# Optimization experiments

Measured on AMD Instinct MI355X. Metric: run time of the kernel, lower is better.

Reference implementation:

```python
import jax, jax.numpy as jnp
import numpy as np

NUM_HEADS = 8
ALPHA = 4.0
KSIZE = 5


def _pow_relu(x, p):
    # relu(x) ** p, safe for x<=0 (avoids 0**p grad NaNs wrt p)
    pos = x > 0
    xs = jnp.where(pos, x, 1.0)
    return jnp.where(pos, xs ** p, 0.0)


def setup_inputs() -> dict:
    key = jax.random.key(0)
    ks = jax.random.split(key, 10)
    B, N, C = 16, 3136, 512
    hd = C // NUM_HEADS
    s = 0.02
    return {
        "x": jax.random.normal(ks[0], (B, N, C), jnp.float32),
        "qg_w": jax.random.normal(ks[1], (C, 2 * C), jnp.float32) * s,
        "kv_w": jax.random.normal(ks[2], (C, 2 * C), jnp.float32) * s,
        "proj_w": jax.random.normal(ks[3], (C, C), jnp.float32) * s,
        "proj_b": jax.random.normal(ks[4], (C,), jnp.float32) * s,
        "pos_enc": jax.random.normal(ks[5], (1, N, C), jnp.float32) * s,
        "scale_p": jax.random.normal(ks[6], (1, 1, C), jnp.float32) * s,
        "power_p": jax.random.normal(ks[7], (1, NUM_HEADS, 1, hd), jnp.float32) * s,
        "dwc_w": jax.random.normal(ks[8], (hd, 1, KSIZE, KSIZE), jnp.float32) * s,
        "dwc_b": jax.random.normal(ks[9], (hd,), jnp.float32) * s,
        "H": 56,
        "W": 56,
    }


def _forward(x, qg_w, kv_w, proj_w, proj_b, pos_enc, scale_p, power_p, dwc_w, dwc_b, H, W):
    B, N, C = x.shape
    nh = NUM_HEADS
    hd = C // nh
    n = N  # sr_ratio == 1

    qg = x @ qg_w                      # [B,N,2C]
    q, g = qg[..., :C], qg[..., C:]
    kv = x @ kv_w                      # [B,N,2C]
    k, v = kv[..., :C], kv[..., C:]
    k = k + pos_enc

    scale = jax.nn.softplus(scale_p)   # [1,1,C]
    q = q / scale
    k = k / scale

    def heads(t):  # [B,N,C] -> [B,nh,N,hd]
        return t.reshape(B, -1, nh, hd).transpose(0, 2, 1, 3)

    q, k, v = heads(q), heads(k), heads(v)

    power = 1.0 + ALPHA * jax.nn.sigmoid(power_p)  # [1,nh,1,hd]
    q_pos = _pow_relu(q, power)
    q_neg = _pow_relu(-q, power)
    q_sim = jnp.concatenate([q_pos, q_neg], -1)    # [B,nh,N,2hd]
    q_opp = jnp.concatenate([q_neg, q_pos], -1)
    kf = jnp.concatenate([_pow_relu(k, power), _pow_relu(-k, power)], -1)  # [B,nh,n,2hd]

    v1, v2 = kf.shape[-1] // 4, None  # v chunks below
    v1, v2 = jnp.split(v, 2, axis=-1)               # each [B,nh,n,hd/2]

    km = kf.mean(axis=2)                            # [B,nh,2hd]
    inv_n = 1.0 / n

    def branch(qf, vv):
        z = 1.0 / (jnp.einsum('bhnd,bhd->bhn', qf, km) + 1e-6)
        kv_ = jnp.einsum('bhnd,bhne->bhde', kf, vv) * inv_n   # (n^-0.5)*(n^-0.5)
        return jnp.einsum('bhnd,bhde->bhne', qf, kv_) * z[..., None]

    x_sim = branch(q_sim, v1)
    x_opp = branch(q_opp, v2)
    xo = jnp.concatenate([x_sim, x_opp], -1)        # [B,nh,N,hd]
    xo = xo.transpose(0, 2, 1, 3).reshape(B, N, C)

    # depthwise conv residual on v
    vimg = v.reshape(B * nh, H, W, hd).transpose(0, 3, 1, 2)  # [B*nh,hd,H,W]
    pad = KSIZE // 2
    vd = jax.lax.conv_general_dilated(
        vimg, dwc_w, window_strides=(1, 1), padding=((pad, pad), (pad, pad)),
        feature_group_count=hd) + dwc_b[None, :, None, None]
    vd = vd.reshape(B, C, N).transpose(0, 2, 1)     # [B,N,C]

    out = (xo + vd) * g
    return out @ proj_w + proj_b


def reference(x, qg_w, kv_w, proj_w, proj_b, pos_enc, scale_p, power_p, dwc_w, dwc_b, H, W):
    return _forward(x, qg_w, kv_w, proj_w, proj_b, pos_enc, scale_p, power_p, dwc_w, dwc_b, H, W)
```

## Files before the change

kernel.cpp:

```cpp
#include <hip/hip_runtime.h>
#include <math.h>

typedef unsigned short ushort;
typedef __attribute__((ext_vector_type(8))) short short8v;
typedef __attribute__((ext_vector_type(4))) short short4v;
typedef __attribute__((ext_vector_type(4))) float float4v;
typedef __attribute__((ext_vector_type(8))) __bf16 bf16x8;

#define NHEADS 8
#define NPOS 3136
#define MROWS 50176
#define KDIM 512

__device__ __forceinline__ ushort f2bf(float f) {
  union { float f; unsigned u; } x; x.f = f;
  unsigned r = x.u + 0x7fffu + ((x.u >> 16) & 1u);
  return (ushort)(r >> 16);
}
__device__ __forceinline__ float bf2f(ushort h) {
  union { unsigned u; float f; } x; x.u = ((unsigned)h) << 16; return x.f;
}

__device__ __forceinline__ float4v mfma16(short8v a, short8v b, float4v c) {
  return __builtin_amdgcn_mfma_f32_16x16x32_bf16(
      __builtin_bit_cast(bf16x8, a), __builtin_bit_cast(bf16x8, b), c, 0, 0, 0);
}

__device__ __forceinline__ void glds16(const void* g, void* l) {
  __builtin_amdgcn_global_load_lds(
      (const __attribute__((address_space(1))) unsigned int*)g,
      (__attribute__((address_space(3))) unsigned int*)l, 16, 0, 0);
}

__device__ __forceinline__ float fexp2(float x) {
  float r; asm("v_exp_f32 %0, %1" : "=v"(r) : "v"(x)); return r;
}
__device__ __forceinline__ float flog2(float x) {
  float r; asm("v_log_f32 %0, %1" : "=v"(r) : "v"(x)); return r;
}

__global__ __launch_bounds__(512) void prep_kernel(const float* __restrict__ scale_p,
                                                   const float* __restrict__ power_p,
                                                   float* __restrict__ scinv,
                                                   float* __restrict__ pwr)
{
  int t = threadIdx.x;
  if (t < KDIM) {
    scinv[t] = 1.f / log1pf(expf(scale_p[t]));
    pwr[t]   = 1.f + 4.f / (1.f + expf(-power_p[t]));
  }
}

__global__ __launch_bounds__(256) void cvt_x_kernel(const float* __restrict__ x,
                                                    ushort* __restrict__ xb)
{
  const size_t i = ((size_t)blockIdx.x * 256 + threadIdx.x) * 4;
  float4v v = *(const float4v*)(x + i);
  short4v o = { (short)f2bf(v[0]), (short)f2bf(v[1]), (short)f2bf(v[2]), (short)f2bf(v[3]) };
  *(short4v*)(xb + i) = o;
}

__global__ __launch_bounds__(256) void transpose_w_kernel(const float* __restrict__ src,
                                                          ushort* __restrict__ dst,
                                                          int K, int N)
{
  __shared__ float tile[32][33];
  const int t = threadIdx.x, tx = t & 31, ty = t >> 5;
  const int nb = blockIdx.x * 32, kb = blockIdx.y * 32;
  #pragma unroll
  for (int i = 0; i < 4; i++)
    tile[ty + i*8][tx] = src[(size_t)(kb + ty + i*8) * N + nb + tx];
  __syncthreads();
  #pragma unroll
  for (int i = 0; i < 4; i++)
    dst[(size_t)(nb + ty + i*8) * K + kb + tx] = f2bf(tile[tx][ty + i*8]);
}

__global__ __launch_bounds__(256) void transpose_pe_kernel(const float* __restrict__ src,
                                                           float* __restrict__ dst)
{
  __shared__ float tile[32][33];
  const int t = threadIdx.x, tx = t & 31, ty = t >> 5;
  const int nb = blockIdx.x * 32, kb = blockIdx.y * 32;
  #pragma unroll
  for (int i = 0; i < 4; i++)
    tile[ty + i*8][tx] = src[(size_t)(kb + ty + i*8) * 512 + nb + tx];
  __syncthreads();
  #pragma unroll
  for (int i = 0; i < 4; i++)
    dst[(size_t)(nb + ty + i*8) * NPOS + kb + tx] = tile[tx][ty + i*8];
}

__global__ __launch_bounds__(512, 6) void gemm_bf16_kernel(
    const ushort* __restrict__ A, const ushort* __restrict__ Bt, int mode,
    const float* __restrict__ scinv, const float* __restrict__ pwr,
    const float* __restrict__ pos_enc, const float* __restrict__ bias,
    float* __restrict__ outf, ushort* __restrict__ outb0, ushort* __restrict__ outb1,
    int nbx_shift)
{
  __shared__ ushort As[3][128*32];
  __shared__ ushort Bs[3][128*32];
  const int t = threadIdx.x;
  const int wave = t >> 6, lane = t & 63;

  const int nwg = (int)(gridDim.x * gridDim.y);
  const int lid = (int)(blockIdx.y * gridDim.x + blockIdx.x);
  const int nlid = (lid & 7) * (nwg >> 3) + (lid >> 3);
  const int bx = nlid & ((1 << nbx_shift) - 1);
  const int by = nlid >> nbx_shift;
  const int m0 = ((mode == 3) ? bx : by) * 128;
  const int n0 = ((mode == 3) ? by : bx) * 128;

  const int wm = wave >> 2, wn = wave & 3;
  const int lm = lane & 15, q = lane >> 4;

  const int srow = t >> 2;
  const int lc = ((t & 3) ^ (srow & 3) ^ ((srow >> 2) & 3)) * 8;
  const ushort* gA = A  + (size_t)(m0 + srow) * KDIM + lc;
  const ushort* gB = Bt + (size_t)(n0 + srow) * KDIM + lc;

  const int pc = (q ^ (lm & 3) ^ ((lm >> 2) & 3)) * 8;
  const int arow = wm * 64 + lm;
  const int brow = wn * 32 + lm;

  float4v acc[4][2];
  #pragma unroll
  for (int i = 0; i < 4; i++)
    #pragma unroll
    for (int j = 0; j < 2; j++) { float4v z = {0.f,0.f,0.f,0.f}; acc[i][j] = z; }

  glds16(gA,      &As[0][t*8]);
  glds16(gB,      &Bs[0][t*8]);
  glds16(gA + 32, &As[1][t*8]);
  glds16(gB + 32, &Bs[1][t*8]);

  #pragma unroll
  for (int kt = 0; kt < 16; kt++) {
    if (kt < 15) asm volatile("s_waitcnt vmcnt(2)" ::: "memory");
    else         asm volatile("s_waitcnt vmcnt(0)" ::: "memory");
    __builtin_amdgcn_sched_barrier(0);
    __builtin_amdgcn_s_barrier();
    if (kt + 2 < 16) {
      const int nb = (kt + 2) % 3;
      glds16(gA + (kt + 2) * 32, &As[nb][t*8]);
      glds16(gB + (kt + 2) * 32, &Bs[nb][t*8]);
    }
    const int cb = kt % 3;
    short8v a[4], b[2];
    #pragma unroll
    for (int i = 0; i < 4; i++)
      a[i] = *(const short8v*)&As[cb][(arow + i*16) * 32 + pc];
    #pragma unroll
    for (int j = 0; j < 2; j++)
      b[j] = *(const short8v*)&Bs[cb][(brow + j*16) * 32 + pc];
    __builtin_amdgcn_s_setprio(1);
    #pragma unroll
    for (int i = 0; i < 4; i++)
      #pragma unroll
      for (int j = 0; j < 2; j++)
        acc[i][j] = mfma16(a[i], b[j], acc[i][j]);
    __builtin_amdgcn_s_setprio(0);
  }

  const int rq = (lane >> 4) * 4;
  if (mode == 3) {
    #pragma unroll
    for (int i = 0; i < 4; i++) {
      const int of0 = m0 + wm * 64 + i * 16 + rq;
      #pragma unroll
      for (int j = 0; j < 2; j++) {
        const int gn = n0 + wn * 32 + j * 16;
        const int bb = gn / NPOS;
        const int nn = gn - bb * NPOS + lm;
        #pragma unroll
        for (int r = 0; r < 4; r++) {
          const int o = of0 + r;
          const float val = acc[i][j][r];
          if (o < 512) {
            const int h = o >> 6, d = o & 63;
            const float sv = (val + pos_enc[(size_t)o * NPOS + nn]) * scinv[o];
            const float pw = pwr[o];
            const float aq = fabsf(sv);
            const float f = fexp2(pw * flog2(aq));
            const ushort fb = f2bf(f);
            ushort* kr = outb0 + ((size_t)((bb << 3) + h) * 128 + 2 * d) * NPOS + nn;
            kr[0]    = (sv > 0.f) ? fb : (ushort)0;
            kr[NPOS] = (sv < 0.f) ? fb : (ushort)0;
          } else {
            const int ov = o - 512;
            const int h = ov >> 6, e = ov & 63;
            outb1[((size_t)((bb << 3) + h) * 64 + e) * NPOS + nn] = f2bf(val);
          }
        }
      }
    }
  } else {
    #pragma unroll
    for (int i = 0; i < 4; i++) {
      #pragma unroll
      for (int r = 0; r < 4; r++) {
        const int grow = m0 + wm * 64 + i * 16 + rq + r;
        const int bb = grow / NPOS;
        const int nn = grow - bb * NPOS;
        #pragma unroll
        for (int j = 0; j < 2; j++) {
          const int gcol = n0 + wn * 32 + j * 16 + lm;
          const float val = acc[i][j][r];
          if (mode == 2) {
            outf[(size_t)grow * 512 + gcol] = val + bias[gcol];
          } else if (gcol < 512) {
            const float sv = val * scinv[gcol];
            const float pw = pwr[gcol];
            const float aq = fabsf(sv);
            const float f = fexp2(pw * flog2(aq));
            const unsigned fb = (unsigned)f2bf(f);
            unsigned pack = 0;
            if (sv > 0.f)      pack = fb;
            else if (sv < 0.f) pack = fb << 16;
            const int h = gcol >> 6, d = gcol & 63;
            unsigned* qrow = (unsigned*)(outb0 + (((size_t)((bb << 3) + h) * NPOS + nn) << 7));
            qrow[d] = pack;
          } else {
            const int c2 = gcol - 512;
            outb1[(size_t)grow * 512 + c2] = f2bf(val);
          }
        }
      }
    }
  }
}

#define RSPLIT 7
#define RK 448
__global__ __launch_bounds__(256, 4) void reduce_kv_kernel(
    const ushort* __restrict__ KFt, const ushort* __restrict__ Vt,
    float* __restrict__ pkv, float* __restrict__ pkm)
{
  __shared__ ushort As[3][128*32];
  __shared__ ushort Bs[3][64*32];
  const int sp = blockIdx.x, bh = blockIdx.y;
  const int t = threadIdx.x;
  const int wave = t >> 6, lane = t & 63;
  const int wm = wave >> 1, wn = wave & 1;
  const int lm = lane & 15, q = lane >> 4;

  const int r0 = t >> 2;
  const int lc = ((t & 3) ^ (r0 & 3) ^ ((r0 >> 2) & 3)) * 8;
  const ushort* gA = KFt + ((size_t)bh * 128 + r0) * NPOS + sp * RK + lc;
  const ushort* gB = Vt  + ((size_t)bh * 64  + r0) * NPOS + sp * RK + lc;
  const size_t A64 = (size_t)64 * NPOS;

  const int pc = (q ^ (lm & 3) ^ ((lm >> 2) & 3)) * 8;
  const int arow = wm * 64 + lm;
  const int brow = wn * 32 + lm;

  float4v acc[4][2], accK[4];
  #pragma unroll
  for (int i = 0; i < 4; i++) {
    #pragma unroll
    for (int j = 0; j < 2; j++) { float4v z = {0.f,0.f,0.f,0.f}; acc[i][j] = z; }
    float4v z = {0.f,0.f,0.f,0.f}; accK[i] = z;
  }
  short8v bk;
  #pragma unroll
  for (int c = 0; c < 8; c++) bk[c] = (short)((lm == 0) ? 0x3F80 : 0);

  glds16(gA,            &As[0][t*8]);
  glds16(gA + A64,      &As[0][2048 + t*8]);
  glds16(gB,            &Bs[0][t*8]);
  glds16(gA + 32,       &As[1][t*8]);
  glds16(gA + A64 + 32, &As[1][2048 + t*8]);
  glds16(gB + 32,       &Bs[1][t*8]);

  #pragma unroll
  for (int kt = 0; kt < 14; kt++) {
    if (kt < 13) asm volatile("s_waitcnt vmcnt(3)" ::: "memory");
    else         asm volatile("s_waitcnt vmcnt(0)" ::: "memory");
    __builtin_amdgcn_sched_barrier(0);
    __builtin_amdgcn_s_barrier();
    if (kt + 2 < 14) {
      const int nb = (kt + 2) % 3;
      const int off = (kt + 2) * 32;
      glds16(gA + off,       &As[nb][t*8]);
      glds16(gA + A64 + off, &As[nb][2048 + t*8]);
      glds16(gB + off,       &Bs[nb][t*8]);
    }
    const int cb = kt % 3;
    short8v a[4], b[2];
    #pragma unroll
    for (int i = 0; i < 4; i++)
      a[i] = *(const short8v*)&As[cb][(arow + i*16) * 32 + pc];
    #pragma unroll
    for (int j = 0; j < 2; j++)
      b[j] = *(const short8v*)&Bs[cb][(brow + j*16) * 32 + pc];
    #pragma unroll
    for (int i = 0; i < 4; i++)
      #pragma unroll
      for (int j = 0; j < 2; j++)
        acc[i][j] = mfma16(a[i], b[j], acc[i][j]);
    if (wn == 0) {
      #pragma unroll
      for (int i = 0; i < 4; i++)
        accK[i] = mfma16(a[i], bk, accK[i]);
    }
  }

  const int rq = q * 4;
  float* op = pkv + (((size_t)sp * 128 + bh) << 13);
  #pragma unroll
  for (int i = 0; i < 4; i++)
    #pragma unroll
    for (int j = 0; j < 2; j++)
      #pragma unroll
      for (int r = 0; r < 4; r++)
        op[(size_t)(wm*64 + i*16 + rq + r) * 64 + wn*32 + j*16 + lm] = acc[i][j][r];
  if (wn == 0 && lm == 0) {
    float* kp = pkm + (((size_t)sp * 128 + bh) << 7);
    #pragma unroll
    for (int i = 0; i < 4; i++)
      #pragma unroll
      for (int r = 0; r < 4; r++)
        kp[wm*64 + i*16 + rq + r] = accK[i][r];
  }
}

__global__ __launch_bounds__(256) void reduce_final_kernel(
    const float* __restrict__ pkv, const float* __restrict__ pkm,
    ushort* __restrict__ Kt)
{
  const int bh = blockIdx.x, t = threadIdx.x;
  const float inv_n = 1.f / (float)NPOS;
  for (int i = t; i < 8192; i += 256) {
    float s = 0.f;
    #pragma unroll
    for (int sp = 0; sp < RSPLIT; sp++) s += pkv[((size_t)(sp*128 + bh) << 13) + i];
    const int d = i >> 6, e = i & 63;
    const int dd = (e < 32) ? d : (d ^ 1);
    Kt[((size_t)bh*80 + e)*128 + dd] = f2bf(s * inv_n);
  }
  if (t < 128) {
    float s = 0.f;
    #pragma unroll
    for (int sp = 0; sp < RSPLIT; sp++) s += pkm[((size_t)(sp*128 + bh) << 7) + t];
    const ushort b = f2bf(s * inv_n);
    Kt[((size_t)bh*80 + 64)*128 + t] = b;
    Kt[((size_t)bh*80 + 65)*128 + (t ^ 1)] = b;
  }
  for (int i = t; i < 14*128; i += 256) Kt[((size_t)bh*80 + 66)*128 + i] = 0;
}

__global__ __launch_bounds__(256) void attn_mfma_kernel(
    const ushort* __restrict__ QS, const ushort* __restrict__ Kt,
    ushort* __restrict__ XO)
{
  __shared__ ushort qs_s[128*128];
  __shared__ ushort kv_s[80*128];
  const int t = threadIdx.x, wave = t >> 6, lane = t & 63;
  const int bh = blockIdx.y;
  const int n0 = blockIdx.x * 128;

  const ushort* ksrc = Kt + (size_t)bh * 80 * 128;
  #pragma unroll
  for (int j = 0; j < 5; j++) {
    const int elem = (j*4096 + wave*1024) >> 1;
    glds16(ksrc + elem + lane*8, kv_s + elem);
  }
  const ushort* qsrc = QS + ((size_t)bh * NPOS + n0) * 128;
  #pragma unroll
  for (int j = 0; j < 8; j++) {
    const int elem = (j*4096 + wave*1024) >> 1;
    glds16(qsrc + elem + lane*8, qs_s + elem);
  }
  __syncthreads();

  const int lm = lane & 15, q8 = (lane >> 4) * 8;
  float4v acc[2][5];
  #pragma unroll
  for (int i = 0; i < 2; i++)
    #pragma unroll
    for (int j = 0; j < 5; j++) { float4v z = {0.f,0.f,0.f,0.f}; acc[i][j] = z; }

  #pragma unroll
  for (int ks = 0; ks < 4; ks++) {
    short8v a[2], b[5];
    #pragma unroll
    for (int i = 0; i < 2; i++)
      a[i] = *(const short8v*)&qs_s[(wave*32 + i*16 + lm)*128 + ks*32 + q8];
    #pragma unroll
    for (int j = 0; j < 5; j++)
      b[j] = *(const short8v*)&kv_s[(j*16 + lm)*128 + ks*32 + q8];
    #pragma unroll
    for (int i = 0; i < 2; i++)
      #pragma unroll
      for (int j = 0; j < 5; j++)
        acc[i][j] = mfma16(a[i], b[j], acc[i][j]);
  }

  const int rq = (lane >> 4) * 4;
  #pragma unroll
  for (int i = 0; i < 2; i++) {
    #pragma unroll
    for (int r = 0; r < 4; r++) {
      const int n = n0 + wave*32 + i*16 + rq + r;
      const float dsim = __shfl(acc[i][4][r], lane & 48);
      const float dopp = __shfl(acc[i][4][r], (lane & 48) | 1);
      const float zs = 1.f / (dsim + 1e-6f);
      const float zo = 1.f / (dopp + 1e-6f);
      if (n < NPOS) {
        ushort* orow = XO + (((size_t)bh * NPOS + n) << 6);
        #pragma unroll
        for (int j = 0; j < 4; j++)
          orow[j*16 + lm] = f2bf(acc[i][j][r] * ((j < 2) ? zs : zo));
      }
    }
  }
}

__global__ __launch_bounds__(256) void conv_combine_kernel(
    const ushort* __restrict__ Vt, const ushort* __restrict__ XO,
    const ushort* __restrict__ g, const float* __restrict__ dwc_w,
    const float* __restrict__ dwc_b, ushort* __restrict__ cmb)
{
  __shared__ ushort vs[6*60*68];
  const int t = threadIdx.x;
  const int bh = blockIdx.y, b = bh >> 3, h = bh & 7;
  const int y0 = blockIdx.x * 2;

  for (int i = t; i < 6*64*4; i += 256) {
    const int c = i & 63, rem = i >> 6;
    const int ry = rem >> 2, hs = rem & 3;
    const int xs = (hs < 2) ? hs : hs + 56;
    vs[(ry*60 + xs)*68 + c] = 0;
  }
  for (int idx = t; idx < 672; idx += 256) {
    const int cgry = idx / 7;
    const int j = idx - cgry * 7;
    const int ry = cgry >> 4, c0 = (cgry & 15) * 4;
    const int yy = y0 - 2 + ry;
    short8v v0 = {0,0,0,0,0,0,0,0}, v1 = v0, v2 = v0, v3 = v0;
    if (yy >= 0 && yy < 56) {
      const ushort* src = &Vt[((size_t)bh*64 + c0)*NPOS + yy*56 + j*8];
      v0 = *(const short8v*)(src);
      v1 = *(const short8v*)(src + NPOS);
      v2 = *(const short8v*)(src + 2*NPOS);
      v3 = *(const short8v*)(src + 3*NPOS);
    }
    ushort* dst = &vs[(ry*60 + j*8 + 2)*68 + c0];
    #pragma unroll
    for (int e = 0; e < 8; e++) {
      short4v p = { v0[e], v1[e], v2[e], v3[e] };
      *(short4v*)(dst + e*68) = p;
    }
  }
  __syncthreads();

  const int c = t & 63, xg = t >> 6;
  float w[25];
  #pragma unroll
  for (int i = 0; i < 25; i++) w[i] = dwc_w[c*25 + i];
  const float bias = dwc_b[c];

  float acc[2][14];
  #pragma unroll
  for (int y = 0; y < 2; y++)
    #pragma unroll
    for (int xi = 0; xi < 14; xi++) acc[y][xi] = bias;

  #pragma unroll
  for (int r = 0; r < 6; r++) {
    float rv[18];
    const ushort* row = &vs[(r*60 + xg*14)*68 + c];
    #pragma unroll
    for (int xl = 0; xl < 18; xl++) rv[xl] = bf2f(row[xl*68]);
    #pragma unroll
    for (int y = 0; y < 2; y++) {
      const int ky = r - y;
      if (ky >= 0 && ky < 5) {
        #pragma unroll
        for (int xl = 0; xl < 18; xl++) {
          #pragma unroll
          for (int kx = 0; kx < 5; kx++) {
            const int xi = xl - kx;
            if (xi >= 0 && xi < 14)
              acc[y][xi] = fmaf(w[ky*5 + kx], rv[xl], acc[y][xi]);
          }
        }
      }
    }
  }

  #pragma unroll
  for (int y = 0; y < 2; y++) {
    const int yo = y0 + y;
    #pragma unroll
    for (int xi = 0; xi < 14; xi++) {
      const int n = yo*56 + xg*14 + xi;
      const float xov = bf2f(XO[(((size_t)bh*NPOS + n) << 6) + c]);
      const size_t nat = ((size_t)b*NPOS + n)*512 + h*64 + c;
      cmb[nat] = f2bf((xov + acc[y][xi]) * bf2f(g[nat]));
    }
  }
}

extern "C" void kernel_launch(void* const* d_in, const int* in_sizes, int n_in,
                              void* d_out, int out_size, void* d_ws, size_t ws_size,
                              hipStream_t stream)
{
  const float* x       = (const float*)d_in[0];
  const float* qg_w    = (const float*)d_in[1];
  const float* kv_w    = (const float*)d_in[2];
  const float* proj_w  = (const float*)d_in[3];
  const float* proj_b  = (const float*)d_in[4];
  const float* pos_enc = (const float*)d_in[5];
  const float* scale_p = (const float*)d_in[6];
  const float* power_p = (const float*)d_in[7];
  const float* dwc_w   = (const float*)d_in[8];
  const float* dwc_b   = (const float*)d_in[9];
  float* out = (float*)d_out;

  const size_t MCs = (size_t)MROWS * 512;
  ushort* xbf = (ushort*)d_ws;
  ushort* KQ  = xbf + MCs;
  ushort* Vt  = KQ + 2*MCs + 8192;
  ushort* Kt  = Vt + MCs;
  ushort* wqg = Kt + (size_t)128*80*128;
  ushort* wkv = wqg + (size_t)1024*512;
  ushort* wpj = wkv + (size_t)1024*512;
  float* pkv  = (float*)(wpj + (size_t)512*512);
  float* pkm  = pkv + (size_t)RSPLIT*128*8192;
  float* scinv= pkm + (size_t)RSPLIT*128*128;
  float* pwr  = scinv + 512;
  const size_t need = (size_t)((char*)(pwr + 512) - (char*)d_ws);
  if (ws_size < need) return;

  ushort* XOb = xbf;
  ushort* cmb = KQ;
  ushort* gbuf = (ushort*)out;
  float* peT = (float*)d_out + 13000000;

  prep_kernel<<<1, 512, 0, stream>>>(scale_p, power_p, scinv, pwr);
  cvt_x_kernel<<<(int)(MCs/4/256), 256, 0, stream>>>(x, xbf);
  transpose_w_kernel<<<dim3(32,16), 256, 0, stream>>>(qg_w,   wqg, 512, 1024);
  transpose_w_kernel<<<dim3(32,16), 256, 0, stream>>>(kv_w,   wkv, 512, 1024);
  transpose_w_kernel<<<dim3(16,16), 256, 0, stream>>>(proj_w, wpj, 512, 512);
  transpose_pe_kernel<<<dim3(16,98), 256, 0, stream>>>(pos_enc, peT);

  gemm_bf16_kernel<<<dim3(8, MROWS/128), 512, 0, stream>>>(
      wkv, xbf, 3, scinv, pwr, peT, nullptr, nullptr, KQ, Vt, 3);
  reduce_kv_kernel<<<dim3(RSPLIT, 128), 256, 0, stream>>>(KQ, Vt, pkv, pkm);
  reduce_final_kernel<<<128, 256, 0, stream>>>(pkv, pkm, Kt);
  gemm_bf16_kernel<<<dim3(8, MROWS/128), 512, 0, stream>>>(
      xbf, wqg, 0, scinv, pwr, nullptr, nullptr, nullptr, KQ, gbuf, 3);
  attn_mfma_kernel<<<dim3(25, 128), 256, 0, stream>>>(KQ, Kt, XOb);
  conv_combine_kernel<<<dim3(28, 128), 256, 0, stream>>>(Vt, XOb, gbuf, dwc_w, dwc_b, cmb);
  gemm_bf16_kernel<<<dim3(4, MROWS/128), 512, 0, stream>>>(
      cmb, wpj, 2, nullptr, nullptr, nullptr, proj_b, out, nullptr, nullptr, 2);
}
```

Before: 615.4 us.

## Fuse linear-attention apply into the QG GEMM epilogue via shared-memory Q tile

The q-feature epilogue of the QG GEMM now writes its power-relu features into a swizzled LDS tile instead of global memory. The same block then runs the small MFMA against the reduced KV/normaliser matrix read directly from global, and writes the normalised attention output. This removes the separate attention kernel and the global round trip of the expanded q features. In exchange the GEMM gains a heavier epilogue with extra barriers and uncached global B-operand loads, which may raise register pressure. Buffer aliasing is reassigned so the output and combine buffers do not overlap the inputs.

After: 661.8 us. 7.5% more time.

```diff
diff --git a/kernel.cpp b/kernel.cpp
--- a/kernel.cpp
+++ b/kernel.cpp
@@ -96,10 +96,9 @@
     const float* __restrict__ scinv, const float* __restrict__ pwr,
     const float* __restrict__ pos_enc, const float* __restrict__ bias,
     float* __restrict__ outf, ushort* __restrict__ outb0, ushort* __restrict__ outb1,
-    int nbx_shift)
-{
-  __shared__ ushort As[3][128*32];
-  __shared__ ushort Bs[3][128*32];
+    const ushort* __restrict__ KtG, int nbx_shift)
+{
+  __shared__ ushort smem[24576];
   const int t = threadIdx.x;
   const int wave = t >> 6, lane = t & 63;
 
@@ -129,10 +128,10 @@
     #pragma unroll
     for (int j = 0; j < 2; j++) { float4v z = {0.f,0.f,0.f,0.f}; acc[i][j] = z; }
 
-  glds16(gA,      &As[0][t*8]);
-  glds16(gB,      &Bs[0][t*8]);
-  glds16(gA + 32, &As[1][t*8]);
-  glds16(gB + 32, &Bs[1][t*8]);
+  glds16(gA,      &smem[t*8]);
+  glds16(gB,      &smem[12288 + t*8]);
+  glds16(gA + 32, &smem[4096 + t*8]);
+  glds16(gB + 32, &smem[12288 + 4096 + t*8]);
 
   #pragma unroll
   for (int kt = 0; kt < 16; kt++) {
@@ -142,17 +141,17 @@
     __builtin_amdgcn_s_barrier();
     if (kt + 2 < 16) {
       const int nb = (kt + 2) % 3;
-      glds16(gA + (kt + 2) * 32, &As[nb][t*8]);
-      glds16(gB + (kt + 2) * 32, &Bs[nb][t*8]);
+      glds16(gA + (kt + 2) * 32, &smem[nb*4096 + t*8]);
+      glds16(gB + (kt + 2) * 32, &smem[12288 + nb*4096 + t*8]);
     }
     const int cb = kt % 3;
     short8v a[4], b[2];
     #pragma unroll
     for (int i = 0; i < 4; i++)
-      a[i] = *(const short8v*)&As[cb][(arow + i*16) * 32 + pc];
+      a[i] = *(const short8v*)&smem[cb*4096 + (arow + i*16) * 32 + pc];
     #pragma unroll
     for (int j = 0; j < 2; j++)
-      b[j] = *(const short8v*)&Bs[cb][(brow + j*16) * 32 + pc];
+      b[j] = *(const short8v*)&smem[12288 + cb*4096 + (brow + j*16) * 32 + pc];
     __builtin_amdgcn_s_setprio(1);
     #pragma unroll
     for (int i = 0; i < 4; i++)
@@ -194,6 +193,71 @@
         }
       }
     }
+  } else if (mode == 0 && bx < 4) {
+    unsigned* qs32 = (unsigned*)smem;
+    __syncthreads();
+    #pragma unroll
+    for (int hsub = 0; hsub < 2; hsub++) {
+      if ((wn >> 1) == hsub) {
+        #pragma unroll
+        for (int i = 0; i < 4; i++) {
+          #pragma unroll
+          for (int j = 0; j < 2; j++) {
+            const int gcol = n0 + wn * 32 + j * 16 + lm;
+            const int dl = (wn & 1) * 32 + j * 16 + lm;
+            const float si = scinv[gcol];
+            const float pw = pwr[gcol];
+            #pragma unroll
+            for (int r = 0; r < 4; r++) {
+              const int row = wm * 64 + i * 16 + rq + r;
+              const float sv = acc[i][j][r] * si;
+              const float aq = fabsf(sv);
+              const float f = fexp2(pw * flog2(aq));
+              const unsigned fb = (unsigned)f2bf(f);
+              unsigned pack = 0;
+              if (sv > 0.f)      pack = fb;
+              else if (sv < 0.f) pack = fb << 16;
+              qs32[row * 64 + (dl ^ ((row & 7) << 3))] = pack;
+            }
+          }
+        }
+      }
+      __syncthreads();
+      const int head = 2 * bx + hsub;
+      const int row0 = wave * 16;
+      const int growW = m0 + row0;
+      const int bbW = growW / NPOS;
+      const int nnW = growW - bbW * NPOS;
+      const int bhW = (bbW << 3) + head;
+      const ushort* ktb = KtG + (size_t)bhW * 80 * 128;
+      float4v accA[5];
+      #pragma unroll
+      for (int j = 0; j < 5; j++) { float4v z = {0.f,0.f,0.f,0.f}; accA[j] = z; }
+      const int rowA = row0 + lm;
+      #pragma unroll
+      for (int ks = 0; ks < 4; ks++) {
+        const int c0 = (ks * 16 + q * 4) ^ ((rowA & 7) << 3);
+        short8v av = *(const short8v*)&smem[(rowA * 64 + c0) * 2];
+        #pragma unroll
+        for (int j = 0; j < 5; j++) {
+          short8v bv = *(const short8v*)&ktb[(size_t)(j * 16 + lm) * 128 + ks * 32 + q * 8];
+          accA[j] = mfma16(av, bv, accA[j]);
+        }
+      }
+      #pragma unroll
+      for (int r = 0; r < 4; r++) {
+        const float dsim = __shfl(accA[4][r], lane & 48);
+        const float dopp = __shfl(accA[4][r], (lane & 48) | 1);
+        const float zs = 1.f / (dsim + 1e-6f);
+        const float zo = 1.f / (dopp + 1e-6f);
+        const int n = nnW + rq + r;
+        ushort* orow = outb0 + (((size_t)bhW * NPOS + n) << 6);
+        #pragma unroll
+        for (int j = 0; j < 4; j++)
+          orow[j * 16 + lm] = f2bf(accA[j][r] * ((j < 2) ? zs : zo));
+      }
+      __syncthreads();
+    }
   } else {
     #pragma unroll
     for (int i = 0; i < 4; i++) {
@@ -208,18 +272,6 @@
           const float val = acc[i][j][r];
           if (mode == 2) {
             outf[(size_t)grow * 512 + gcol] = val + bias[gcol];
-          } else if (gcol < 512) {
-            const float sv = val * scinv[gcol];
-            const float pw = pwr[gcol];
-            const float aq = fabsf(sv);
-            const float f = fexp2(pw * flog2(aq));
-            const unsigned fb = (unsigned)f2bf(f);
-            unsigned pack = 0;
-            if (sv > 0.f)      pack = fb;
-            else if (sv < 0.f) pack = fb << 16;
-            const int h = gcol >> 6, d = gcol & 63;
-            unsigned* qrow = (unsigned*)(outb0 + (((size_t)((bb << 3) + h) * NPOS + nn) << 7));
-            qrow[d] = pack;
           } else {
             const int c2 = gcol - 512;
             outb1[(size_t)grow * 512 + c2] = f2bf(val);
@@ -347,73 +399,6 @@
     Kt[((size_t)bh*80 + 65)*128 + (t ^ 1)] = b;
   }
   for (int i = t; i < 14*128; i += 256) Kt[((size_t)bh*80 + 66)*128 + i] = 0;
-}
-
-__global__ __launch_bounds__(256) void attn_mfma_kernel(
-    const ushort* __restrict__ QS, const ushort* __restrict__ Kt,
-    ushort* __restrict__ XO)
-{
-  __shared__ ushort qs_s[128*128];
-  __shared__ ushort kv_s[80*128];
-  const int t = threadIdx.x, wave = t >> 6, lane = t & 63;
-  const int bh = blockIdx.y;
-  const int n0 = blockIdx.x * 128;
-
-  const ushort* ksrc = Kt + (size_t)bh * 80 * 128;
-  #pragma unroll
-  for (int j = 0; j < 5; j++) {
-    const int elem = (j*4096 + wave*1024) >> 1;
-    glds16(ksrc + elem + lane*8, kv_s + elem);
-  }
-  const ushort* qsrc = QS + ((size_t)bh * NPOS + n0) * 128;
-  #pragma unroll
-  for (int j = 0; j < 8; j++) {
-    const int elem = (j*4096 + wave*1024) >> 1;
-    glds16(qsrc + elem + lane*8, qs_s + elem);
-  }
-  __syncthreads();
-
-  const int lm = lane & 15, q8 = (lane >> 4) * 8;
-  float4v acc[2][5];
-  #pragma unroll
-  for (int i = 0; i < 2; i++)
-    #pragma unroll
-    for (int j = 0; j < 5; j++) { float4v z = {0.f,0.f,0.f,0.f}; acc[i][j] = z; }
-
-  #pragma unroll
-  for (int ks = 0; ks < 4; ks++) {
-    short8v a[2], b[5];
-    #pragma unroll
-    for (int i = 0; i < 2; i++)
-      a[i] = *(const short8v*)&qs_s[(wave*32 + i*16 + lm)*128 + ks*32 + q8];
-    #pragma unroll
-    for (int j = 0; j < 5; j++)
-      b[j] = *(const short8v*)&kv_s[(j*16 + lm)*128 + ks*32 + q8];
-    #pragma unroll
-    for (int i = 0; i < 2; i++)
-      #pragma unroll
-      for (int j = 0; j < 5; j++)
-        acc[i][j] = mfma16(a[i], b[j], acc[i][j]);
-  }
-
-  const int rq = (lane >> 4) * 4;
-  #pragma unroll
-  for (int i = 0; i < 2; i++) {
-    #pragma unroll
-    for (int r = 0; r < 4; r++) {
-      const int n = n0 + wave*32 + i*16 + rq + r;
-      const float dsim = __shfl(acc[i][4][r], lane & 48);
-      const float dopp = __shfl(acc[i][4][r], (lane & 48) | 1);
-      const float zs = 1.f / (dsim + 1e-6f);
-      const float zo = 1.f / (dopp + 1e-6f);
-      if (n < NPOS) {
-        ushort* orow = XO + (((size_t)bh * NPOS + n) << 6);
-        #pragma unroll
-        for (int j = 0; j < 4; j++)
-          orow[j*16 + lm] = f2bf(acc[i][j][r] * ((j < 2) ? zs : zo));
-      }
-    }
-  }
 }
 
 __global__ __launch_bounds__(256) void conv_combine_kernel(
@@ -533,8 +518,8 @@
   const size_t need = (size_t)((char*)(pwr + 512) - (char*)d_ws);
   if (ws_size < need) return;
 
-  ushort* XOb = xbf;
-  ushort* cmb = KQ;
+  ushort* XOb = KQ;
+  ushort* cmb = KQ + MCs;
   ushort* gbuf = (ushort*)out;
   float* peT = (float*)d_out + 13000000;
 
@@ -546,13 +531,12 @@
   transpose_pe_kernel<<<dim3(16,98), 256, 0, stream>>>(pos_enc, peT);
 
   gemm_bf16_kernel<<<dim3(8, MROWS/128), 512, 0, stream>>>(
-      wkv, xbf, 3, scinv, pwr, peT, nullptr, nullptr, KQ, Vt, 3);
+      wkv, xbf, 3, scinv, pwr, peT, nullptr, nullptr, KQ, Vt, nullptr, 3);
   reduce_kv_kernel<<<dim3(RSPLIT, 128), 256, 0, stream>>>(KQ, Vt, pkv, pkm);
   reduce_final_kernel<<<128, 256, 0, stream>>>(pkv, pkm, Kt);
   gemm_bf16_kernel<<<dim3(8, MROWS/128), 512, 0, stream>>>(
-      xbf, wqg, 0, scinv, pwr, nullptr, nullptr, nullptr, KQ, gbuf, 3);
-  attn_mfma_kernel<<<dim3(25, 128), 256, 0, stream>>>(KQ, Kt, XOb);
+      xbf, wqg, 0, scinv, pwr, nullptr, nullptr, nullptr, XOb, gbuf, Kt, 3);
   conv_combine_kernel<<<dim3(28, 128), 256, 0, stream>>>(Vt, XOb, gbuf, dwc_w, dwc_b, cmb);
   gemm_bf16_kernel<<<dim3(4, MROWS/128), 512, 0, stream>>>(
-      cmb, wpj, 2, nullptr, nullptr, nullptr, proj_b, out, nullptr, nullptr, 2);
-}
+      cmb, wpj, 2, nullptr, nullptr, nullptr, proj_b, out, nullptr, nullptr, nullptr, 2);
+}
```
